# Performance work log

Measured on AMD Instinct MI355X. Metric: run time of the kernel, lower is better.

Reference implementation:

```python
import jax, jax.numpy as jnp
import numpy as np

FS = 512.0
SEQ_LEN = 2048
PHA_N, AMP_N, N_BINS = 50, 30, 18


def _bands():
    # PAC.calc_bands_pha: mid in linspace(2,20,50), band = [mid - mid/4, mid + mid/4]
    pha_mid = np.linspace(2.0, 20.0, PHA_N)
    pha = np.stack([pha_mid * 0.75, pha_mid * 1.25], axis=1)
    # amp_end_hz = int(min(fs/2/(1+0.8) - 1, 160)) = 141 for fs=512
    amp_end = float(int(min(FS / 2.0 / 1.8 - 1.0, 160.0)))
    # PAC.calc_bands_amp: mid in linspace(60,141,30), band = [mid - mid/8, mid + mid/8]
    amp_mid = np.linspace(60.0, amp_end, AMP_N)
    amp = np.stack([amp_mid * 0.875, amp_mid * 1.125], axis=1)
    return np.concatenate([pha, amp], axis=0).astype(np.float32)  # (80, 2)


def setup_inputs() -> dict:
    key = jax.random.key(0)
    x = jax.random.normal(key, (2, 8, 1, SEQ_LEN), dtype=jnp.float32)
    return {"x": x}


def _pac(x):
    # x: (B, C, S, T)
    B, C, S, T = x.shape
    bands = jnp.asarray(_bands())                        # (F, 2), F = 80
    freqs = jnp.abs(jnp.fft.fftfreq(T, d=1.0 / FS)).astype(jnp.float32)
    # zero-phase brick-wall bandpass masks, one per band
    mask = ((freqs[None, :] >= bands[:, :1]) & (freqs[None, :] <= bands[:, 1:2])).astype(jnp.complex64)  # (F, T)
    # Hilbert analytic-signal multiplier (T even)
    half = T // 2
    h = jnp.zeros((T,), jnp.float32).at[0].set(1.0).at[half].set(1.0).at[1:half].set(2.0)
    Xf = jnp.fft.fft(x, axis=-1)                          # (B, C, S, T) complex
    analytic = jnp.fft.ifft(Xf[:, :, :, None, :] * mask[None, None, None] * h.astype(jnp.complex64), axis=-1)  # (B, C, S, F, T)
    # transpose segments/bands as in forward (x.transpose(2, 3))
    pha = jnp.angle(analytic).transpose(0, 1, 3, 2, 4)[:, :, :PHA_N]   # (B, C, P, S, T)
    amp = jnp.abs(analytic).transpose(0, 1, 3, 2, 4)[:, :, -AMP_N:]    # (B, C, A, S, T)
    edge = T // 8
    pha = pha[..., edge:-edge]
    amp = amp[..., edge:-edge]                                          # Tt = T - 2*edge
    # Modulation index: bin phases into 18 bins over [-pi, pi], mean amp per bin
    width = 2.0 * jnp.pi / N_BINS
    idx = jnp.clip(jnp.floor((pha + jnp.pi) / width), 0, N_BINS - 1).astype(jnp.int32)
    oh = jax.nn.one_hot(idx, N_BINS, dtype=amp.dtype)                   # (B, C, P, S, Tt, K)
    counts = oh.sum(axis=-2)                                            # (B, C, P, S, K)
    sums = jnp.einsum('bcpstk,bcast->bcpask', oh, amp)                  # (B, C, P, A, S, K)
    means = sums / jnp.maximum(counts[:, :, :, None], 1e-9)
    probs = means / jnp.maximum(means.sum(axis=-1, keepdims=True), 1e-9)
    log_nb = jnp.log(jnp.float32(N_BINS))
    # MI = (log K + sum_k p log p) / log K  (KL divergence from uniform, normalized)
    mi = (log_nb + (probs * jnp.log(probs + 1e-9)).sum(axis=-1)) / log_nb  # (B, C, P, A, S)
    return mi.mean(axis=-1)                                             # (B, C, P, A)


def reference(x):
    return _pac(x)
```

## Files before the change

kernel.cpp:

```cpp
#include <hip/hip_runtime.h>
#include <hip/hip_bf16.h>
#include <math.h>

#ifndef M_PI
#define M_PI 3.14159265358979323846
#endif

#define T 2048
#define EDGE 256
#define TT 1536
#define PHA_N 50
#define AMP_N 30
#define NBANDS 80
#define NBINS 18
#define NBC 16
#define FMAX 768
#define NCH 16
#define CHLEN (T / NCH)

typedef __attribute__((ext_vector_type(8))) short short8;
typedef __attribute__((ext_vector_type(8))) _Float16 half8;
typedef __attribute__((ext_vector_type(16))) float float16;

__device__ __forceinline__ void band_range(int band, int* fl, int* fh) {
    double lo, hi;
    if (band < PHA_N) {
        double mid = 2.0 + (double)band * (18.0 / 49.0);
        lo = (double)(float)(mid * 0.75);
        hi = (double)(float)(mid * 1.25);
    } else {
        int j = band - PHA_N;
        double mid = 60.0 + (double)j * (81.0 / 29.0);
        lo = (double)(float)(mid * 0.875);
        hi = (double)(float)(mid * 1.125);
    }
    int l = (int)ceil(lo * 4.0);
    int h = (int)floor(hi * 4.0);
    if (l < 1) l = 1;
    if (h > FMAX - 1) h = FMAX - 1;
    *fl = l; *fh = h;
}

__global__ void dft_kernel(const float* __restrict__ x, double* __restrict__ Xp) {
    __shared__ float xs[CHLEN];
    const int bc = blockIdx.x;
    const int fb = blockIdx.y;
    const int ch = blockIdx.z;
    const int tid = threadIdx.x;
    const int t0 = ch * CHLEN;
    if (tid < CHLEN) xs[tid] = x[bc * T + t0 + tid];
    __syncthreads();
    const int f = fb * 256 + tid;
    const double om = 2.0 * M_PI / (double)T;
    double s, c;
    sincos(om * (double)(f & (T - 1)), &s, &c);
    const double wR = c, wI = -s;
    double curR[2], curI[2], accR[2], accI[2];
    #pragma unroll
    for (int h = 0; h < 2; ++h) {
        sincos(om * (double)((f * (t0 + h * 64)) & (T - 1)), &s, &c);
        curR[h] = c; curI[h] = -s;
        accR[h] = 0.0; accI[h] = 0.0;
    }
    #pragma unroll 2
    for (int t = 0; t < 64; ++t) {
        #pragma unroll
        for (int h = 0; h < 2; ++h) {
            double v = (double)xs[t + h * 64];
            accR[h] += v * curR[h];
            accI[h] += v * curI[h];
            double nR = curR[h] * wR - curI[h] * wI;
            double nI = curR[h] * wI + curI[h] * wR;
            curR[h] = nR; curI[h] = nI;
        }
    }
    const size_t o = (size_t)((ch * NBC + bc) * FMAX + f) * 2;
    Xp[o + 0] = accR[0] + accR[1];
    Xp[o + 1] = accI[0] + accI[1];
}

#define NJ 3
__global__ void band_kernel(const double* __restrict__ Xp,
                            unsigned char* __restrict__ idx_buf,
                            _Float16* __restrict__ Abuf) {
    __shared__ float sXr[164];
    __shared__ float sXi[164];
    const int bc = blockIdx.x;
    const int band = (NBANDS - 1) - blockIdx.y;
    const int half = blockIdx.z;
    const int tid = threadIdx.x;
    int fl, fh;
    band_range(band, &fl, &fh);
    const int nb = fh - fl + 1;
    const int t00 = tid + half * 768 + EDGE;

    for (int i = tid; i < nb; i += 256) {
        const int f = fl + i;
        double r = 0.0, im = 0.0;
        #pragma unroll
        for (int c = 0; c < NCH; ++c) {
            const size_t o = (size_t)((c * NBC + bc) * FMAX + f) * 2;
            r += Xp[o]; im += Xp[o + 1];
        }
        sXr[i] = (float)r; sXi[i] = (float)im;
    }
    __syncthreads();

    float curR[NJ], curI[NJ], wR[NJ], wI[NJ], accR[NJ], accI[NJ];
    {
        const float omf = (float)(2.0 * M_PI / (double)T);
        float s, c;
        sincosf(omf * (float)((fl * t00) & (T - 1)), &s, &c);
        curR[0] = c; curI[0] = s;
        sincosf(omf * (float)(t00 & (T - 1)), &s, &c);
        wR[0] = c; wI[0] = s;
        sincosf(omf * (float)((fl << 8) & (T - 1)), &s, &c);
        const float scR = c, scI = s;
        const float swc = 0.70710678f;
        #pragma unroll
        for (int j = 1; j < NJ; ++j) {
            curR[j] = curR[j-1] * scR - curI[j-1] * scI;
            curI[j] = curR[j-1] * scI + curI[j-1] * scR;
            wR[j] = wR[j-1] * swc - wI[j-1] * swc;
            wI[j] = wR[j-1] * swc + wI[j-1] * swc;
        }
        #pragma unroll
        for (int j = 0; j < NJ; ++j) { accR[j] = 0.0f; accI[j] = 0.0f; }
    }
    #pragma unroll 2
    for (int i = 0; i < nb; ++i) {
        const float Xr = sXr[i], Xi = sXi[i];
        #pragma unroll
        for (int j = 0; j < NJ; ++j) {
            accR[j] += Xr * curR[j] - Xi * curI[j];
            accI[j] += Xr * curI[j] + Xi * curR[j];
            float nR = curR[j] * wR[j] - curI[j] * wI[j];
            float nI = curR[j] * wI[j] + curI[j] * wR[j];
            curR[j] = nR; curI[j] = nI;
        }
    }

    if (band < PHA_N) {
        const float widthf = (float)(2.0 * M_PI / (double)NBINS);
        const float pif = (float)M_PI;
        #pragma unroll
        for (int j = 0; j < NJ; ++j) {
            const int trel = tid + j * 256 + half * 768;
            float pha = atan2f(accI[j], accR[j]);
            int b = (int)floorf((pha + pif) / widthf);
            if (b < 0) b = 0;
            if (b > NBINS - 1) b = NBINS - 1;
            idx_buf[(size_t)(bc * PHA_N + band) * TT + trel] = (unsigned char)b;
        }
    } else {
        const int a = band - PHA_N;
        #pragma unroll
        for (int j = 0; j < NJ; ++j) {
            const int trel = tid + j * 256 + half * 768;
            float amp = sqrtf(accR[j] * accR[j] + accI[j] * accI[j]) * (2.0f / (float)T);
            Abuf[(size_t)(bc * 32 + a) * TT + trel] = (_Float16)amp;
            if (band == NBANDS - 1)
                Abuf[(size_t)(bc * 32 + 30) * TT + trel] = (_Float16)1.0f;
        }
    }
}

__global__ void mi_kernel(const unsigned char* __restrict__ idx_buf,
                          const _Float16* __restrict__ Abuf,
                          float* __restrict__ out) {
    __shared__ unsigned int sidx_s[TT / 4];
    __shared__ float cpart[4][32][NBINS];
    const int blk = blockIdx.x;
    const int bc = blk / PHA_N;
    const int p = blk % PHA_N;
    const int tid = threadIdx.x;
    const int wave = tid >> 6;
    const int lane = tid & 63;

    for (int i = tid; i < TT / 4; i += 256)
        sidx_s[i] = ((const unsigned int*)(idx_buf + (size_t)(bc * PHA_N + p) * TT))[i];
    __syncthreads();

    const int n = lane & 31;
    const int kq = lane >> 5;
    const half8* arow = (const half8*)(Abuf + (size_t)(bc * 32 + n) * TT
                                       + wave * 384 + kq * 8);
    float16 acc = {0.0f};
    #pragma unroll 4
    for (int ks = 0; ks < 24; ++ks) {
        const half8 a = arow[ks * 2];
        const int w0 = wave * 96 + ks * 4 + kq * 2;
        const unsigned int lo = sidx_s[w0];
        const unsigned int hi = sidx_s[w0 + 1];
        short8 bs;
        bs[0] = ((lo & 0xffu) == (unsigned)n) ? (short)0x3C00 : (short)0;
        bs[1] = (((lo >> 8) & 0xffu) == (unsigned)n) ? (short)0x3C00 : (short)0;
        bs[2] = (((lo >> 16) & 0xffu) == (unsigned)n) ? (short)0x3C00 : (short)0;
        bs[3] = ((lo >> 24) == (unsigned)n) ? (short)0x3C00 : (short)0;
        bs[4] = ((hi & 0xffu) == (unsigned)n) ? (short)0x3C00 : (short)0;
        bs[5] = (((hi >> 8) & 0xffu) == (unsigned)n) ? (short)0x3C00 : (short)0;
        bs[6] = (((hi >> 16) & 0xffu) == (unsigned)n) ? (short)0x3C00 : (short)0;
        bs[7] = ((hi >> 24) == (unsigned)n) ? (short)0x3C00 : (short)0;
        const half8 b = __builtin_bit_cast(half8, bs);
        acc = __builtin_amdgcn_mfma_f32_32x32x16_f16(a, b, acc, 0, 0, 0);
    }

    if (n < NBINS) {
        #pragma unroll
        for (int r = 0; r < 16; ++r) {
            const int row = (r & 3) + 8 * (r >> 2) + 4 * kq;
            if (row < 31) cpart[wave][row][n] = acc[r];
        }
    }
    __syncthreads();

    if (tid < AMP_N) {
        const int a = tid;
        double m[NBINS], tot = 0.0;
        #pragma unroll
        for (int k = 0; k < NBINS; ++k) {
            double cnt = (double)(cpart[0][30][k] + cpart[1][30][k]
                                + cpart[2][30][k] + cpart[3][30][k]);
            double denom = cnt > 1e-9 ? cnt : 1e-9;
            double s = (double)(cpart[0][a][k] + cpart[1][a][k]
                              + cpart[2][a][k] + cpart[3][a][k]);
            m[k] = s / denom;
            tot += m[k];
        }
        double dt = tot > 1e-9 ? tot : 1e-9;
        double accm = 0.0;
        #pragma unroll
        for (int k = 0; k < NBINS; ++k) {
            double pr = m[k] / dt;
            accm += pr * log(pr + 1e-9);
        }
        const double lognb = log((double)NBINS);
        out[(size_t)blk * AMP_N + a] = (float)((lognb + accm) / lognb);
    }
}

extern "C" void kernel_launch(void* const* d_in, const int* in_sizes, int n_in,
                              void* d_out, int out_size, void* d_ws, size_t ws_size,
                              hipStream_t stream) {
    const float* x = (const float*)d_in[0];
    float* out = (float*)d_out;
    char* ws = (char*)d_ws;
    unsigned char* idx_buf = (unsigned char*)ws;
    _Float16* Abuf = (_Float16*)(ws + 1228800);
    double* Xp = (double*)(ws + 2801664);

    dft_kernel<<<dim3(NBC, FMAX / 256, NCH), 256, 0, stream>>>(x, Xp);
    band_kernel<<<dim3(NBC, NBANDS, 2), 256, 0, stream>>>(Xp, idx_buf, Abuf);
    mi_kernel<<<NBC * PHA_N, 256, 0, stream>>>(idx_buf, Abuf, out);
}
```

Baseline: 114.5 us.

## Compute band-limited inverse DFTs via shared prefix sums over frequency

The band kernel no longer evaluates a separate inverse DFT per band. Each block handles 64 time samples, and 12 waves each accumulate a frequency chunk of one shared running sum. Snapshots are taken at every band edge, then per-wave carries are combined so each band's signal is the difference of two prefix values. This drops the redundant per-band work on overlapping frequency ranges, at the cost of a sort, atomics, serialized carry accumulation, and extra float32 cancellation error from differencing large prefix sums.

```diff
diff --git a/kernel.cpp b/kernel.cpp
--- a/kernel.cpp
+++ b/kernel.cpp
@@ -17,6 +17,10 @@
 #define FMAX 768
 #define NCH 16
 #define CHLEN (T / NCH)
+#define NW 12
+#define CS 53
+#define TPB (NW * 64)
+#define NEV (2 * NBANDS)
 
 typedef __attribute__((ext_vector_type(8))) short short8;
 typedef __attribute__((ext_vector_type(8))) _Float16 half8;
@@ -79,90 +83,116 @@
     Xp[o + 1] = accI[0] + accI[1];
 }
 
-#define NJ 3
-__global__ void band_kernel(const double* __restrict__ Xp,
-                            unsigned char* __restrict__ idx_buf,
-                            _Float16* __restrict__ Abuf) {
-    __shared__ float sXr[164];
-    __shared__ float sXi[164];
+__global__ __launch_bounds__(TPB)
+void band_kernel(const double* __restrict__ Xp,
+                 unsigned char* __restrict__ idx_buf,
+                 _Float16* __restrict__ Abuf) {
+    __shared__ float sXr[640], sXi[640];
+    __shared__ float snapR[NEV][64];
+    __shared__ float snapI[NEV][64];
+    __shared__ float totR[NW][64], totI[NW][64];
+    __shared__ float carR[NW][64], carI[NW][64];
+    __shared__ int bfl[NBANDS], bfh[NBANDS];
+    __shared__ int ef[NEV];
+    __shared__ short srt_f[NEV];
+    __shared__ unsigned char srt_s[NEV];
+    __shared__ int cstart[NW];
     const int bc = blockIdx.x;
-    const int band = (NBANDS - 1) - blockIdx.y;
-    const int half = blockIdx.z;
+    const int tg = blockIdx.y;
     const int tid = threadIdx.x;
-    int fl, fh;
-    band_range(band, &fl, &fh);
-    const int nb = fh - fl + 1;
-    const int t00 = tid + half * 768 + EDGE;
-
-    for (int i = tid; i < nb; i += 256) {
-        const int f = fl + i;
+    const int wave = tid >> 6, lane = tid & 63;
+    const int t = tg * 64 + lane + EDGE;
+
+    for (int i = tid; i < 634; i += TPB) {
+        const int f = i + 1;
         double r = 0.0, im = 0.0;
         #pragma unroll
         for (int c = 0; c < NCH; ++c) {
             const size_t o = (size_t)((c * NBC + bc) * FMAX + f) * 2;
             r += Xp[o]; im += Xp[o + 1];
         }
-        sXr[i] = (float)r; sXi[i] = (float)im;
-    }
-    __syncthreads();
-
-    float curR[NJ], curI[NJ], wR[NJ], wI[NJ], accR[NJ], accI[NJ];
+        sXr[f] = (float)r; sXi[f] = (float)im;
+    }
+    if (tid < NBANDS) { int fl, fh; band_range(tid, &fl, &fh); bfl[tid] = fl; bfh[tid] = fh; }
+    if (tid < NW) cstart[tid] = NEV;
+    __syncthreads();
+    if (tid < NEV) ef[tid] = (tid & 1) ? bfh[tid >> 1] : bfl[tid >> 1] - 1;
+    __syncthreads();
+    if (tid < NEV) {
+        const int fe = ef[tid];
+        int rank = 0;
+        for (int j = 0; j < NEV; ++j) {
+            const int fj = ef[j];
+            rank += (fj < fe || (fj == fe && j < tid)) ? 1 : 0;
+        }
+        srt_f[rank] = (short)fe;
+        srt_s[rank] = (unsigned char)tid;
+        atomicMin(&cstart[(fe - 1) / CS], rank);
+    }
+    __syncthreads();
+
+    const int g0 = wave * CS + 1;
+    const int g1 = min(g0 + CS - 1, 634);
+    int ptr = cstart[wave];
+    int nf = (ptr < NEV) ? (int)srt_f[ptr] : 10000;
+    const float omf = (float)(2.0 * M_PI / (double)T);
+    float ss, cc;
+    sincosf(omf * (float)(t & (T - 1)), &ss, &cc);
+    float Er, Ei;
+    { float s0, c0; sincosf(omf * (float)(((g0 - 1) * t) & (T - 1)), &s0, &c0);
+      Er = c0; Ei = s0; }
+    float Pr = 0.0f, Pi = 0.0f;
+    for (int g = g0; g <= g1; ++g) {
+        const float nEr = Er * cc - Ei * ss;
+        const float nEi = Er * ss + Ei * cc;
+        Er = nEr; Ei = nEi;
+        const float Xr = sXr[g], Xi = sXi[g];
+        Pr += Xr * Er - Xi * Ei;
+        Pi += Xr * Ei + Xi * Er;
+        while (g == nf) {
+            const int slot = srt_s[ptr];
+            snapR[slot][lane] = Pr;
+            snapI[slot][lane] = Pi;
+            ++ptr;
+            nf = (ptr < NEV) ? (int)srt_f[ptr] : 10000;
+        }
+    }
+    totR[wave][lane] = Pr; totI[wave][lane] = Pi;
+    __syncthreads();
     {
-        const float omf = (float)(2.0 * M_PI / (double)T);
-        float s, c;
-        sincosf(omf * (float)((fl * t00) & (T - 1)), &s, &c);
-        curR[0] = c; curI[0] = s;
-        sincosf(omf * (float)(t00 & (T - 1)), &s, &c);
-        wR[0] = c; wI[0] = s;
-        sincosf(omf * (float)((fl << 8) & (T - 1)), &s, &c);
-        const float scR = c, scI = s;
-        const float swc = 0.70710678f;
-        #pragma unroll
-        for (int j = 1; j < NJ; ++j) {
-            curR[j] = curR[j-1] * scR - curI[j-1] * scI;
-            curI[j] = curR[j-1] * scI + curI[j-1] * scR;
-            wR[j] = wR[j-1] * swc - wI[j-1] * swc;
-            wI[j] = wR[j-1] * swc + wI[j-1] * swc;
-        }
-        #pragma unroll
-        for (int j = 0; j < NJ; ++j) { accR[j] = 0.0f; accI[j] = 0.0f; }
-    }
-    #pragma unroll 2
-    for (int i = 0; i < nb; ++i) {
-        const float Xr = sXr[i], Xi = sXi[i];
-        #pragma unroll
-        for (int j = 0; j < NJ; ++j) {
-            accR[j] += Xr * curR[j] - Xi * curI[j];
-            accI[j] += Xr * curI[j] + Xi * curR[j];
-            float nR = curR[j] * wR[j] - curI[j] * wI[j];
-            float nI = curR[j] * wI[j] + curI[j] * wR[j];
-            curR[j] = nR; curI[j] = nI;
-        }
-    }
-
-    if (band < PHA_N) {
-        const float widthf = (float)(2.0 * M_PI / (double)NBINS);
-        const float pif = (float)M_PI;
-        #pragma unroll
-        for (int j = 0; j < NJ; ++j) {
-            const int trel = tid + j * 256 + half * 768;
-            float pha = atan2f(accI[j], accR[j]);
+        float cr = 0.0f, ci = 0.0f;
+        for (int w = 0; w < wave; ++w) { cr += totR[w][lane]; ci += totI[w][lane]; }
+        carR[wave][lane] = cr; carI[wave][lane] = ci;
+    }
+    __syncthreads();
+
+    const float widthf = (float)(2.0 * M_PI / (double)NBINS);
+    const float pif = (float)M_PI;
+    for (int o = tid; o < NBANDS * 64; o += TPB) {
+        const int band = o >> 6, tl = o & 63;
+        const int fl = bfl[band], fh = bfh[band];
+        const int clo = (fl - 2) / CS;
+        const int chi = (fh - 1) / CS;
+        const float PloR = snapR[2 * band][tl] + carR[clo][tl];
+        const float PloI = snapI[2 * band][tl] + carI[clo][tl];
+        const float PhiR = snapR[2 * band + 1][tl] + carR[chi][tl];
+        const float PhiI = snapI[2 * band + 1][tl] + carI[chi][tl];
+        const float Sr = PhiR - PloR;
+        const float Si = PhiI - PloI;
+        const int trel = tg * 64 + tl;
+        if (band < PHA_N) {
+            float pha = atan2f(Si, Sr);
             int b = (int)floorf((pha + pif) / widthf);
             if (b < 0) b = 0;
             if (b > NBINS - 1) b = NBINS - 1;
             idx_buf[(size_t)(bc * PHA_N + band) * TT + trel] = (unsigned char)b;
-        }
-    } else {
-        const int a = band - PHA_N;
-        #pragma unroll
-        for (int j = 0; j < NJ; ++j) {
-            const int trel = tid + j * 256 + half * 768;
-            float amp = sqrtf(accR[j] * accR[j] + accI[j] * accI[j]) * (2.0f / (float)T);
-            Abuf[(size_t)(bc * 32 + a) * TT + trel] = (_Float16)amp;
-            if (band == NBANDS - 1)
-                Abuf[(size_t)(bc * 32 + 30) * TT + trel] = (_Float16)1.0f;
-        }
-    }
+        } else {
+            float amp = sqrtf(Sr * Sr + Si * Si) * (2.0f / (float)T);
+            Abuf[(size_t)(bc * 32 + (band - PHA_N)) * TT + trel] = (_Float16)amp;
+        }
+    }
+    if (tid < 64)
+        Abuf[(size_t)(bc * 32 + 30) * TT + tg * 64 + tid] = (_Float16)1.0f;
 }
 
 __global__ void mi_kernel(const unsigned char* __restrict__ idx_buf,
@@ -250,6 +280,6 @@
     double* Xp = (double*)(ws + 2801664);
 
     dft_kernel<<<dim3(NBC, FMAX / 256, NCH), 256, 0, stream>>>(x, Xp);
-    band_kernel<<<dim3(NBC, NBANDS, 2), 256, 0, stream>>>(Xp, idx_buf, Abuf);
+    band_kernel<<<dim3(NBC, TT / 64), TPB, 0, stream>>>(Xp, idx_buf, Abuf);
     mi_kernel<<<NBC * PHA_N, 256, 0, stream>>>(idx_buf, Abuf, out);
 }
```

New measurement: 125.0 us. 1.09x slower.

## Recast band inverse DFT as fp16 MFMA matmul over band masks

Applied to the files above, without the earlier changes.

The per-band scalar twiddle recurrence is replaced by a matrix formulation. Each block takes 32 time samples, builds twiddle-weighted spectra as fp16 B operands, and multiplies them by 0/1 band-mask A operands using 32x32x16 MFMA across all 80 bands at once. The cross-chunk reduction of the partial DFT moves into a separate reduce kernel. The aim is to use matrix cores instead of scalar FMAs, at the cost of fp16 rounding of the spectrum terms, an extra launch, and a large shared-memory reduction.

```diff
diff --git a/kernel.cpp b/kernel.cpp
--- a/kernel.cpp
+++ b/kernel.cpp
@@ -17,6 +17,9 @@
 #define FMAX 768
 #define NCH 16
 #define CHLEN (T / NCH)
+#define BK 640
+#define BWAVES 4
+#define KPW (BK / BWAVES)
 
 typedef __attribute__((ext_vector_type(8))) short short8;
 typedef __attribute__((ext_vector_type(8))) _Float16 half8;
@@ -79,90 +82,142 @@
     Xp[o + 1] = accI[0] + accI[1];
 }
 
-#define NJ 3
-__global__ void band_kernel(const double* __restrict__ Xp,
-                            unsigned char* __restrict__ idx_buf,
-                            _Float16* __restrict__ Abuf) {
-    __shared__ float sXr[164];
-    __shared__ float sXi[164];
+__global__ void reduce_kernel(const double* __restrict__ Xp, float2* __restrict__ Xf) {
+    const int gid = blockIdx.x * 256 + threadIdx.x;
+    double r = 0.0, im = 0.0;
+    #pragma unroll
+    for (int c = 0; c < NCH; ++c) {
+        r  += Xp[((size_t)c * NBC * FMAX + gid) * 2 + 0];
+        im += Xp[((size_t)c * NBC * FMAX + gid) * 2 + 1];
+    }
+    Xf[gid] = make_float2((float)r, (float)im);
+}
+
+__global__ __launch_bounds__(256, 3)
+void band_kernel(const float2* __restrict__ Xf,
+                 unsigned char* __restrict__ idx_buf,
+                 _Float16* __restrict__ Abuf) {
+    __shared__ float uni[2560];
+    __shared__ float cpart[BWAVES][2560];
+    __shared__ int bfl_s[96], bfh_s[96];
     const int bc = blockIdx.x;
-    const int band = (NBANDS - 1) - blockIdx.y;
-    const int half = blockIdx.z;
+    const int tg = blockIdx.y;
     const int tid = threadIdx.x;
-    int fl, fh;
-    band_range(band, &fl, &fh);
-    const int nb = fh - fl + 1;
-    const int t00 = tid + half * 768 + EDGE;
-
-    for (int i = tid; i < nb; i += 256) {
-        const int f = fl + i;
-        double r = 0.0, im = 0.0;
-        #pragma unroll
-        for (int c = 0; c < NCH; ++c) {
-            const size_t o = (size_t)((c * NBC + bc) * FMAX + f) * 2;
-            r += Xp[o]; im += Xp[o + 1];
-        }
-        sXr[i] = (float)r; sXi[i] = (float)im;
-    }
-    __syncthreads();
-
-    float curR[NJ], curI[NJ], wR[NJ], wI[NJ], accR[NJ], accI[NJ];
-    {
-        const float omf = (float)(2.0 * M_PI / (double)T);
-        float s, c;
-        sincosf(omf * (float)((fl * t00) & (T - 1)), &s, &c);
-        curR[0] = c; curI[0] = s;
-        sincosf(omf * (float)(t00 & (T - 1)), &s, &c);
-        wR[0] = c; wI[0] = s;
-        sincosf(omf * (float)((fl << 8) & (T - 1)), &s, &c);
-        const float scR = c, scI = s;
-        const float swc = 0.70710678f;
-        #pragma unroll
-        for (int j = 1; j < NJ; ++j) {
-            curR[j] = curR[j-1] * scR - curI[j-1] * scI;
-            curI[j] = curR[j-1] * scI + curI[j-1] * scR;
-            wR[j] = wR[j-1] * swc - wI[j-1] * swc;
-            wI[j] = wR[j-1] * swc + wI[j-1] * swc;
-        }
-        #pragma unroll
-        for (int j = 0; j < NJ; ++j) { accR[j] = 0.0f; accI[j] = 0.0f; }
-    }
-    #pragma unroll 2
-    for (int i = 0; i < nb; ++i) {
-        const float Xr = sXr[i], Xi = sXi[i];
-        #pragma unroll
-        for (int j = 0; j < NJ; ++j) {
-            accR[j] += Xr * curR[j] - Xi * curI[j];
-            accI[j] += Xr * curI[j] + Xi * curR[j];
-            float nR = curR[j] * wR[j] - curI[j] * wI[j];
-            float nI = curR[j] * wI[j] + curI[j] * wR[j];
-            curR[j] = nR; curI[j] = nI;
-        }
-    }
-
-    if (band < PHA_N) {
-        const float widthf = (float)(2.0 * M_PI / (double)NBINS);
-        const float pif = (float)M_PI;
-        #pragma unroll
-        for (int j = 0; j < NJ; ++j) {
-            const int trel = tid + j * 256 + half * 768;
-            float pha = atan2f(accI[j], accR[j]);
+    const int wave = tid >> 6, lane = tid & 63;
+    const int n = lane & 31;
+    const int kq = lane >> 5;
+    const int t = tg * 32 + n + EDGE;
+
+    for (int i = tid; i < BK; i += 256) {
+        const float2 v = Xf[bc * FMAX + i + 1];
+        uni[i] = v.x; uni[1280 + i] = v.y;
+    }
+    if (tid < 96) {
+        int fl = 1, fh = 0;
+        if (tid < NBANDS) band_range(tid, &fl, &fh);
+        bfl_s[tid] = fl; bfh_s[tid] = fh;
+    }
+    __syncthreads();
+
+    const int fl0 = bfl_s[n],      fh0 = bfh_s[n];
+    const int fl1 = bfl_s[32 + n], fh1 = bfh_s[32 + n];
+    const int fl2 = bfl_s[64 + n], fh2 = bfh_s[64 + n];
+
+    const float omf = (float)(2.0 * M_PI / (double)T);
+    float sw, cw;
+    sincosf(omf * (float)(t & (T - 1)), &sw, &cw);
+    float r16c = cw, r16s = sw;
+    #pragma unroll
+    for (int q = 0; q < 4; ++q) {
+        const float nc = r16c * r16c - r16s * r16s;
+        const float ns = 2.0f * r16c * r16s;
+        r16c = nc; r16s = ns;
+    }
+    const int Koff = wave * KPW;
+    const int gg0 = 1 + Koff + kq * 8;
+    float cur0c, cur0s;
+    { float s0, c0; sincosf(omf * (float)((gg0 * t) & (T - 1)), &s0, &c0);
+      cur0c = c0; cur0s = s0; }
+
+    float16 aR0 = {0.0f}, aR1 = {0.0f}, aR2 = {0.0f};
+    float16 aI0 = {0.0f}, aI1 = {0.0f}, aI2 = {0.0f};
+    for (int ks = 0; ks < 10; ++ks) {
+        const int kbase = Koff + kq * 8 + ks * 16;
+        float cc = cur0c, cs = cur0s;
+        half8 bre, bim;
+        #pragma unroll
+        for (int j = 0; j < 8; ++j) {
+            const float Xr = uni[kbase + j];
+            const float Xi = uni[1280 + kbase + j];
+            bre[j] = (_Float16)(Xr * cc - Xi * cs);
+            bim[j] = (_Float16)(Xr * cs + Xi * cc);
+            const float nc = cc * cw - cs * sw;
+            const float ns = cc * sw + cs * cw;
+            cc = nc; cs = ns;
+        }
+        { const float nc = cur0c * r16c - cur0s * r16s;
+          const float ns = cur0c * r16s + cur0s * r16c;
+          cur0c = nc; cur0s = ns; }
+        short8 a0s, a1s, a2s;
+        #pragma unroll
+        for (int j = 0; j < 8; ++j) {
+            const int g = kbase + j + 1;
+            a0s[j] = (g >= fl0 && g <= fh0) ? (short)0x3C00 : (short)0;
+            a1s[j] = (g >= fl1 && g <= fh1) ? (short)0x3C00 : (short)0;
+            a2s[j] = (g >= fl2 && g <= fh2) ? (short)0x3C00 : (short)0;
+        }
+        const half8 a0 = __builtin_bit_cast(half8, a0s);
+        const half8 a1 = __builtin_bit_cast(half8, a1s);
+        const half8 a2 = __builtin_bit_cast(half8, a2s);
+        aR0 = __builtin_amdgcn_mfma_f32_32x32x16_f16(a0, bre, aR0, 0, 0, 0);
+        aI0 = __builtin_amdgcn_mfma_f32_32x32x16_f16(a0, bim, aI0, 0, 0, 0);
+        aR1 = __builtin_amdgcn_mfma_f32_32x32x16_f16(a1, bre, aR1, 0, 0, 0);
+        aI1 = __builtin_amdgcn_mfma_f32_32x32x16_f16(a1, bim, aI1, 0, 0, 0);
+        aR2 = __builtin_amdgcn_mfma_f32_32x32x16_f16(a2, bre, aR2, 0, 0, 0);
+        aI2 = __builtin_amdgcn_mfma_f32_32x32x16_f16(a2, bim, aI2, 0, 0, 0);
+    }
+    __syncthreads();
+
+    #pragma unroll
+    for (int r = 0; r < 16; ++r) {
+        const int row = (r & 3) + 8 * (r >> 2) + 4 * kq;
+        cpart[wave][row * 32 + n] = aR0[r];
+        cpart[wave][(32 + row) * 32 + n] = aR1[r];
+        if (row < 16) cpart[wave][(64 + row) * 32 + n] = aR2[r];
+    }
+    __syncthreads();
+    for (int i = tid; i < 2560; i += 256)
+        uni[i] = cpart[0][i] + cpart[1][i] + cpart[2][i] + cpart[3][i];
+    __syncthreads();
+    #pragma unroll
+    for (int r = 0; r < 16; ++r) {
+        const int row = (r & 3) + 8 * (r >> 2) + 4 * kq;
+        cpart[wave][row * 32 + n] = aI0[r];
+        cpart[wave][(32 + row) * 32 + n] = aI1[r];
+        if (row < 16) cpart[wave][(64 + row) * 32 + n] = aI2[r];
+    }
+    __syncthreads();
+
+    const float widthf = (float)(2.0 * M_PI / (double)NBINS);
+    const float pif = (float)M_PI;
+    for (int i = tid; i < 2560; i += 256) {
+        const int band = i >> 5, nn = i & 31;
+        const float Sre = uni[i];
+        const float Sim = cpart[0][i] + cpart[1][i] + cpart[2][i] + cpart[3][i];
+        const int trel = tg * 32 + nn;
+        if (band < PHA_N) {
+            float pha = atan2f(Sim, Sre);
             int b = (int)floorf((pha + pif) / widthf);
             if (b < 0) b = 0;
             if (b > NBINS - 1) b = NBINS - 1;
             idx_buf[(size_t)(bc * PHA_N + band) * TT + trel] = (unsigned char)b;
-        }
-    } else {
-        const int a = band - PHA_N;
-        #pragma unroll
-        for (int j = 0; j < NJ; ++j) {
-            const int trel = tid + j * 256 + half * 768;
-            float amp = sqrtf(accR[j] * accR[j] + accI[j] * accI[j]) * (2.0f / (float)T);
-            Abuf[(size_t)(bc * 32 + a) * TT + trel] = (_Float16)amp;
-            if (band == NBANDS - 1)
-                Abuf[(size_t)(bc * 32 + 30) * TT + trel] = (_Float16)1.0f;
-        }
-    }
+        } else {
+            float amp = sqrtf(Sre * Sre + Sim * Sim) * (2.0f / (float)T);
+            Abuf[(size_t)(bc * 32 + (band - PHA_N)) * TT + trel] = (_Float16)amp;
+        }
+    }
+    if (tid < 32)
+        Abuf[(size_t)(bc * 32 + 30) * TT + tg * 32 + tid] = (_Float16)1.0f;
 }
 
 __global__ void mi_kernel(const unsigned char* __restrict__ idx_buf,
@@ -248,8 +303,10 @@
     unsigned char* idx_buf = (unsigned char*)ws;
     _Float16* Abuf = (_Float16*)(ws + 1228800);
     double* Xp = (double*)(ws + 2801664);
+    float2* Xf = (float2*)(ws + 5947392);
 
     dft_kernel<<<dim3(NBC, FMAX / 256, NCH), 256, 0, stream>>>(x, Xp);
-    band_kernel<<<dim3(NBC, NBANDS, 2), 256, 0, stream>>>(Xp, idx_buf, Abuf);
+    reduce_kernel<<<NBC * FMAX / 256, 256, 0, stream>>>(Xp, Xf);
+    band_kernel<<<dim3(NBC, TT / 32), 256, 0, stream>>>(Xf, idx_buf, Abuf);
     mi_kernel<<<NBC * PHA_N, 256, 0, stream>>>(idx_buf, Abuf, out);
 }
```

Result: faster. 104.3 us (-8.9%).
